# Optimization experiments

Measured on AMD Instinct MI355X. Metric: run time of the kernel, lower is better.

## Reference

```python
import jax, jax.numpy as jnp
import numpy as np

MASK_VALUE = 1.0e6   # mask_value default in get_interpolation
N_NH = 3             # nh_inter: number of nearest neighbors kept by topk
POWER = 2            # inverse-distance weighting power
CUTOFF_DIST = 0.01   # cutoff_dist: distances clamped below this value


def setup_inputs() -> dict:
    key = jax.random.key(0)
    k1, k2, k3 = jax.random.split(key, 3)
    b, n_l, l, nh, nv, f = 1, 4096, 16, 1, 4, 1
    nh_sz, nt = 9, 16            # neighbor cells per cell; target points per cell
    n = n_l * l                  # 65536 fine-grid points
    K = nh_sz * l * nh           # 144 candidate source points per cell
    x = jax.random.normal(k1, (b, n, nh, nv, f), dtype=jnp.float32)
    mask = jnp.zeros((b, n, nh, nv), dtype=jnp.float32)  # 0 = valid point
    dist = jax.random.uniform(k2, (b, n_l, nt, K), dtype=jnp.float32)
    nh_idx = jax.random.randint(k3, (n_l, nh_sz), 0, n_l)  # neighbor-cell table
    return {"x": x, "mask": mask, "dist": dist, "nh_idx": nh_idx}


def reference(x, mask, dist, nh_idx):
    b, n, nh, nv, f = x.shape            # f == 1 (required by original gather layout)
    _, n_l, nt, K = dist.shape
    l = n // n_l
    # --- get_nh: group fine points into coarse cells, gather neighbor cells ---
    x_c = x.reshape(b, n_l, l * nh * nv * f)
    m_c = mask.reshape(b, n_l, l * nh * nv)
    x_nh = x_c[:, nh_idx].reshape(b, n_l, K, nv, f)      # (b,n_l,K,nv,f)
    mask_nh = m_c[:, nh_idx].reshape(b, n_l, K, nv)      # (b,n_l,K,nv)
    # --- masked distances broadcast over target points and variables ---
    dist_m = dist[:, :, :, :, None] + mask_nh[:, :, None, :, :] * MASK_VALUE  # (b,n_l,nt,K,nv)
    dist_m = jnp.moveaxis(dist_m, 3, -1)                 # (b,n_l,nt,nv,K)
    # --- top-k smallest distances (irregular topk) ---
    neg_vals, idx = jax.lax.top_k(-dist_m, N_NH)
    dist_vals = -neg_vals                                # (b,n_l,nt,nv,N_NH)
    # --- gather selected neighbor features ---
    xh = jnp.moveaxis(x_nh[..., 0], 2, -1)               # (b,n_l,nv,K)
    xh = jnp.broadcast_to(xh[:, :, None], (b, n_l, nt, nv, K))
    x_g = jnp.take_along_axis(xh, idx, axis=-1)          # (b,n_l,nt,nv,N_NH)
    # --- inverse-distance weights ---
    dv = jnp.maximum(dist_vals, CUTOFF_DIST)
    w = 1.0 / dv ** POWER
    w = w / w.sum(axis=-1, keepdims=True)
    x_inter = (x_g * w).sum(axis=-1)                     # (b,n_l,nt,nv)
    return x_inter.reshape(b, n_l * nt, nv, f)
```

## Files before the change

### kernel.cpp

```cpp
#include <hip/hip_runtime.h>

#define N_L   4096
#define NT    16
#define NV    4
#define NHSZ  9
#define KCAND 144
#define MASKV 1.0e6f
#define CUT   0.01f
#define BIG   3.0e38f

__global__ __launch_bounds__(256) void flag_kernel(const float* __restrict__ mask,
                                                   int* __restrict__ flags) {
    int gid  = blockIdx.x * 256 + threadIdx.x;
    int cell = gid >> 6;
    int lane = gid & 63;
    if (cell < N_L) {
        float m = mask[cell * 64 + lane];
        unsigned long long b = __ballot(m != 0.0f);
        if (lane == 0) flags[cell] = (b != 0ULL) ? 1 : 0;
    }
}

__global__ __launch_bounds__(256) void interp_kernel(
    const float* __restrict__ x,
    const float* __restrict__ mask,
    const float* __restrict__ dist,
    const int*   __restrict__ nh_idx,
    const int*   __restrict__ flags,
    float*       __restrict__ out)
{
    const int tid = blockIdx.x * 256 + threadIdx.x;
    const int c   = tid >> 4;

    int  cells[NHSZ];
    bool clean = true;
#pragma unroll
    for (int j = 0; j < NHSZ; ++j) {
        cells[j] = nh_idx[c * NHSZ + j];
        clean &= (flags[cells[j]] == 0);
    }

    const float4* dp = (const float4*)(dist + (size_t)tid * KCAND);
    const float4* xc = (const float4*)x;
    const float4* mc = (const float4*)mask;

    float4 result;

    if (clean) {
        float d0 = BIG, d1 = BIG, d2 = BIG;
        int   i0 = 0,   i1 = 0,   i2 = 0;

#pragma unroll 6
        for (int q = 0; q < KCAND / 4; ++q) {
            float4 dd = dp[q];
            const float de[4] = {dd.x, dd.y, dd.z, dd.w};
            const int kb = q * 4;
#pragma unroll
            for (int e = 0; e < 4; ++e) {
                float d = de[e];
                int   k = kb + e;
                bool c0 = d < d0, c1 = d < d1, c2 = d < d2;
                d2 = c1 ? d1 : (c2 ? d : d2);
                i2 = c1 ? i1 : (c2 ? k : i2);
                d1 = c0 ? d0 : (c1 ? d : d1);
                i1 = c0 ? i0 : (c1 ? k : i1);
                d0 = c0 ? d  : d0;
                i0 = c0 ? k  : i0;
            }
        }

        int j0 = i0 >> 4, p0 = i0 & 15;
        int j1 = i1 >> 4, p1 = i1 & 15;
        int j2 = i2 >> 4, p2 = i2 & 15;
        float4 xa = xc[cells[j0] * 16 + p0];
        float4 xb = xc[cells[j1] * 16 + p1];
        float4 xd = xc[cells[j2] * 16 + p2];

        float v0 = fmaxf(d0, CUT), v1 = fmaxf(d1, CUT), v2 = fmaxf(d2, CUT);
        float w0 = 1.0f / (v0 * v0);
        float w1 = 1.0f / (v1 * v1);
        float w2 = 1.0f / (v2 * v2);
        float inv = 1.0f / (w0 + w1 + w2);

        result.x = (xa.x * w0 + xb.x * w1 + xd.x * w2) * inv;
        result.y = (xa.y * w0 + xb.y * w1 + xd.y * w2) * inv;
        result.z = (xa.z * w0 + xb.z * w1 + xd.z * w2) * inv;
        result.w = (xa.w * w0 + xb.w * w1 + xd.w * w2) * inv;
    } else {
        float sd[NV][3];
        int   si[NV][3];
#pragma unroll
        for (int v = 0; v < NV; ++v) {
            sd[v][0] = sd[v][1] = sd[v][2] = BIG;
            si[v][0] = si[v][1] = si[v][2] = 0;
        }
        for (int q = 0; q < KCAND / 4; ++q) {
            float4 dd = dp[q];
            const float de[4] = {dd.x, dd.y, dd.z, dd.w};
#pragma unroll
            for (int e = 0; e < 4; ++e) {
                int k = q * 4 + e;
                int j = k >> 4, p = k & 15;
                float4 m4 = mc[cells[j] * 16 + p];
                const float me[4] = {m4.x, m4.y, m4.z, m4.w};
#pragma unroll
                for (int v = 0; v < NV; ++v) {
                    float dm = fmaf(me[v], MASKV, de[e]);
                    bool c0 = dm < sd[v][0], c1 = dm < sd[v][1], c2 = dm < sd[v][2];
                    sd[v][2] = c1 ? sd[v][1] : (c2 ? dm : sd[v][2]);
                    si[v][2] = c1 ? si[v][1] : (c2 ? k  : si[v][2]);
                    sd[v][1] = c0 ? sd[v][0] : (c1 ? dm : sd[v][1]);
                    si[v][1] = c0 ? si[v][0] : (c1 ? k  : si[v][1]);
                    sd[v][0] = c0 ? dm : sd[v][0];
                    si[v][0] = c0 ? k  : si[v][0];
                }
            }
        }
        float res[NV];
#pragma unroll
        for (int v = 0; v < NV; ++v) {
            float acc = 0.0f, wsum = 0.0f;
#pragma unroll
            for (int s = 0; s < 3; ++s) {
                int k = si[v][s];
                int j = k >> 4, p = k & 15;
                float xv = x[cells[j] * 64 + p * 4 + v];
                float dv = fmaxf(sd[v][s], CUT);
                float w  = 1.0f / (dv * dv);
                acc  += xv * w;
                wsum += w;
            }
            res[v] = acc / wsum;
        }
        result = make_float4(res[0], res[1], res[2], res[3]);
    }

    ((float4*)out)[tid] = result;
}

extern "C" void kernel_launch(void* const* d_in, const int* in_sizes, int n_in,
                              void* d_out, int out_size, void* d_ws, size_t ws_size,
                              hipStream_t stream) {
    const float* x      = (const float*)d_in[0];
    const float* mask   = (const float*)d_in[1];
    const float* dist   = (const float*)d_in[2];
    const int*   nh_idx = (const int*)d_in[3];
    float*       out    = (float*)d_out;
    int*         flags  = (int*)d_ws;

    flag_kernel<<<(N_L * 64) / 256, 256, 0, stream>>>(mask, flags);

    interp_kernel<<<(N_L * NT) / 256, 256, 0, stream>>>(x, mask, dist, nh_idx,
                                                        flags, out);
}
```

Baseline: 88.40 us.

## Split each row across four lanes with shuffle top-3 merge and inline mask check

Each target row is now handled by four threads instead of one. Each thread scans an interleaved quarter of the 144 candidate distances, and the partial top-3 lists are merged with two xor-shuffle rounds using index tie-breaking. The separate flag kernel is removed: each block loads its four cells' neighbor tables into shared memory and sets a per-cell dirty flag from the mask with shared atomics. The aim is better-coalesced dist loads, more threads in flight and one fewer launch. In exchange, each block re-reads neighbor mask data that overlaps between blocks, and the masked path now walks candidates one scalar at a time per variable.

```diff
diff --git a/kernel.cpp b/kernel.cpp
--- a/kernel.cpp
+++ b/kernel.cpp
@@ -9,16 +9,8 @@
 #define CUT   0.01f
 #define BIG   3.0e38f
 
-__global__ __launch_bounds__(256) void flag_kernel(const float* __restrict__ mask,
-                                                   int* __restrict__ flags) {
-    int gid  = blockIdx.x * 256 + threadIdx.x;
-    int cell = gid >> 6;
-    int lane = gid & 63;
-    if (cell < N_L) {
-        float m = mask[cell * 64 + lane];
-        unsigned long long b = __ballot(m != 0.0f);
-        if (lane == 0) flags[cell] = (b != 0ULL) ? 1 : 0;
-    }
+__device__ __forceinline__ bool lex_lt(float da, int ia, float db, int ib) {
+    return (da < db) || ((da == db) && (ia < ib));
 }
 
 __global__ __launch_bounds__(256) void interp_kernel(
@@ -26,116 +18,121 @@
     const float* __restrict__ mask,
     const float* __restrict__ dist,
     const int*   __restrict__ nh_idx,
-    const int*   __restrict__ flags,
     float*       __restrict__ out)
 {
-    const int tid = blockIdx.x * 256 + threadIdx.x;
-    const int c   = tid >> 4;
+    __shared__ int s_cells[4 * NHSZ];
+    __shared__ int s_dirty[4];
 
-    int  cells[NHSZ];
-    bool clean = true;
+    const int t    = threadIdx.x;
+    const int row0 = blockIdx.x * 64;
+    const int c0   = row0 >> 4;
+
+    if (t < 4) s_dirty[t] = 0;
+    if (t < 4 * NHSZ) s_cells[t] = nh_idx[c0 * NHSZ + t];
+    __syncthreads();
+
 #pragma unroll
-    for (int j = 0; j < NHSZ; ++j) {
-        cells[j] = nh_idx[c * NHSZ + j];
-        clean &= (flags[cells[j]] == 0);
+    for (int i = 0; i < 9; ++i) {
+        int f = t + 256 * i;
+        int e = f >> 6;
+        int w = f & 63;
+        float m = mask[s_cells[e] * 64 + w];
+        if (m != 0.0f) atomicOr(&s_dirty[e / 9], 1);
     }
+    __syncthreads();
 
-    const float4* dp = (const float4*)(dist + (size_t)tid * KCAND);
-    const float4* xc = (const float4*)x;
-    const float4* mc = (const float4*)mask;
+    const int row = row0 + (t >> 2);
+    const int sub = t & 3;
+    const int lc  = (t >> 2) >> 4;
+    const int* cells = &s_cells[lc * NHSZ];
 
-    float4 result;
-
-    if (clean) {
+    if (s_dirty[lc] == 0) {
+        const float4* dp = (const float4*)(dist + (size_t)row * KCAND);
         float d0 = BIG, d1 = BIG, d2 = BIG;
         int   i0 = 0,   i1 = 0,   i2 = 0;
-
-#pragma unroll 6
-        for (int q = 0; q < KCAND / 4; ++q) {
-            float4 dd = dp[q];
+#pragma unroll
+        for (int m = 0; m < 9; ++m) {
+            float4 dd = dp[sub + 4 * m];
             const float de[4] = {dd.x, dd.y, dd.z, dd.w};
-            const int kb = q * 4;
+            const int kb = 4 * sub + 16 * m;
 #pragma unroll
             for (int e = 0; e < 4; ++e) {
                 float d = de[e];
                 int   k = kb + e;
-                bool c0 = d < d0, c1 = d < d1, c2 = d < d2;
-                d2 = c1 ? d1 : (c2 ? d : d2);
-                i2 = c1 ? i1 : (c2 ? k : i2);
-                d1 = c0 ? d0 : (c1 ? d : d1);
-                i1 = c0 ? i0 : (c1 ? k : i1);
-                d0 = c0 ? d  : d0;
-                i0 = c0 ? k  : i0;
+                bool c0_ = d < d0, c1_ = d < d1, c2_ = d < d2;
+                d2 = c1_ ? d1 : (c2_ ? d : d2);
+                i2 = c1_ ? i1 : (c2_ ? k : i2);
+                d1 = c0_ ? d0 : (c1_ ? d : d1);
+                i1 = c0_ ? i0 : (c1_ ? k : i1);
+                d0 = c0_ ? d  : d0;
+                i0 = c0_ ? k  : i0;
             }
         }
 
-        int j0 = i0 >> 4, p0 = i0 & 15;
-        int j1 = i1 >> 4, p1 = i1 & 15;
-        int j2 = i2 >> 4, p2 = i2 & 15;
-        float4 xa = xc[cells[j0] * 16 + p0];
-        float4 xb = xc[cells[j1] * 16 + p1];
-        float4 xd = xc[cells[j2] * 16 + p2];
+#pragma unroll
+        for (int mm = 0; mm < 2; ++mm) {
+            const int msk = 1 << mm;
+            float ed0 = __shfl_xor(d0, msk);
+            float ed1 = __shfl_xor(d1, msk);
+            float ed2 = __shfl_xor(d2, msk);
+            int   ei0 = __shfl_xor(i0, msk);
+            int   ei1 = __shfl_xor(i1, msk);
+            int   ei2 = __shfl_xor(i2, msk);
+            bool cA = lex_lt(d0, i0, ed0, ei0);
+            float lo0d = cA ? d0 : ed0;  int lo0i = cA ? i0 : ei0;
+            float hi0d = cA ? ed0 : d0;  int hi0i = cA ? ei0 : i0;
+            bool cB = lex_lt(d1, i1, ed1, ei1);
+            float lo1d = cB ? d1 : ed1;  int lo1i = cB ? i1 : ei1;
+            float hi1d = cB ? ed1 : d1;  int hi1i = cB ? ei1 : i1;
+            bool cC = lex_lt(d2, i2, ed2, ei2);
+            float lo2d = cC ? d2 : ed2;  int lo2i = cC ? i2 : ei2;
+            bool cD = lex_lt(hi0d, hi0i, lo1d, lo1i);
+            float r1d = cD ? hi0d : lo1d; int r1i = cD ? hi0i : lo1i;
+            float t2d = cD ? lo1d : hi0d; int t2i = cD ? lo1i : hi0i;
+            bool cE = lex_lt(t2d, t2i, lo2d, lo2i);
+            float r2d = cE ? t2d : lo2d;  int r2i = cE ? t2i : lo2i;
+            d0 = lo0d; i0 = lo0i;
+            d1 = r1d;  i1 = r1i;
+            d2 = r2d;  i2 = r2i;
+        }
 
         float v0 = fmaxf(d0, CUT), v1 = fmaxf(d1, CUT), v2 = fmaxf(d2, CUT);
         float w0 = 1.0f / (v0 * v0);
         float w1 = 1.0f / (v1 * v1);
         float w2 = 1.0f / (v2 * v2);
         float inv = 1.0f / (w0 + w1 + w2);
-
-        result.x = (xa.x * w0 + xb.x * w1 + xd.x * w2) * inv;
-        result.y = (xa.y * w0 + xb.y * w1 + xd.y * w2) * inv;
-        result.z = (xa.z * w0 + xb.z * w1 + xd.z * w2) * inv;
-        result.w = (xa.w * w0 + xb.w * w1 + xd.w * w2) * inv;
+        int j0 = i0 >> 4, p0 = i0 & 15;
+        int j1 = i1 >> 4, p1 = i1 & 15;
+        int j2 = i2 >> 4, p2 = i2 & 15;
+        float xa = x[cells[j0] * 64 + p0 * 4 + sub];
+        float xb = x[cells[j1] * 64 + p1 * 4 + sub];
+        float xd = x[cells[j2] * 64 + p2 * 4 + sub];
+        out[row * 4 + sub] = (xa * w0 + xb * w1 + xd * w2) * inv;
     } else {
-        float sd[NV][3];
-        int   si[NV][3];
-#pragma unroll
-        for (int v = 0; v < NV; ++v) {
-            sd[v][0] = sd[v][1] = sd[v][2] = BIG;
-            si[v][0] = si[v][1] = si[v][2] = 0;
+        const float* dr = dist + (size_t)row * KCAND;
+        float d0 = BIG, d1 = BIG, d2 = BIG;
+        int   i0 = 0,   i1 = 0,   i2 = 0;
+        for (int k = 0; k < KCAND; ++k) {
+            int j = k >> 4, p = k & 15;
+            float dm = fmaf(mask[cells[j] * 64 + p * 4 + sub], MASKV, dr[k]);
+            bool c0_ = dm < d0, c1_ = dm < d1, c2_ = dm < d2;
+            d2 = c1_ ? d1 : (c2_ ? dm : d2);
+            i2 = c1_ ? i1 : (c2_ ? k  : i2);
+            d1 = c0_ ? d0 : (c1_ ? dm : d1);
+            i1 = c0_ ? i0 : (c1_ ? k  : i1);
+            d0 = c0_ ? dm : d0;
+            i0 = c0_ ? k  : i0;
         }
-        for (int q = 0; q < KCAND / 4; ++q) {
-            float4 dd = dp[q];
-            const float de[4] = {dd.x, dd.y, dd.z, dd.w};
-#pragma unroll
-            for (int e = 0; e < 4; ++e) {
-                int k = q * 4 + e;
-                int j = k >> 4, p = k & 15;
-                float4 m4 = mc[cells[j] * 16 + p];
-                const float me[4] = {m4.x, m4.y, m4.z, m4.w};
-#pragma unroll
-                for (int v = 0; v < NV; ++v) {
-                    float dm = fmaf(me[v], MASKV, de[e]);
-                    bool c0 = dm < sd[v][0], c1 = dm < sd[v][1], c2 = dm < sd[v][2];
-                    sd[v][2] = c1 ? sd[v][1] : (c2 ? dm : sd[v][2]);
-                    si[v][2] = c1 ? si[v][1] : (c2 ? k  : si[v][2]);
-                    sd[v][1] = c0 ? sd[v][0] : (c1 ? dm : sd[v][1]);
-                    si[v][1] = c0 ? si[v][0] : (c1 ? k  : si[v][1]);
-                    sd[v][0] = c0 ? dm : sd[v][0];
-                    si[v][0] = c0 ? k  : si[v][0];
-                }
-            }
-        }
-        float res[NV];
-#pragma unroll
-        for (int v = 0; v < NV; ++v) {
-            float acc = 0.0f, wsum = 0.0f;
-#pragma unroll
-            for (int s = 0; s < 3; ++s) {
-                int k = si[v][s];
-                int j = k >> 4, p = k & 15;
-                float xv = x[cells[j] * 64 + p * 4 + v];
-                float dv = fmaxf(sd[v][s], CUT);
-                float w  = 1.0f / (dv * dv);
-                acc  += xv * w;
-                wsum += w;
-            }
-            res[v] = acc / wsum;
-        }
-        result = make_float4(res[0], res[1], res[2], res[3]);
+        float v0 = fmaxf(d0, CUT), v1 = fmaxf(d1, CUT), v2 = fmaxf(d2, CUT);
+        float w0 = 1.0f / (v0 * v0);
+        float w1 = 1.0f / (v1 * v1);
+        float w2 = 1.0f / (v2 * v2);
+        float inv = 1.0f / (w0 + w1 + w2);
+        float xa = x[cells[i0 >> 4] * 64 + (i0 & 15) * 4 + sub];
+        float xb = x[cells[i1 >> 4] * 64 + (i1 & 15) * 4 + sub];
+        float xd = x[cells[i2 >> 4] * 64 + (i2 & 15) * 4 + sub];
+        out[row * 4 + sub] = (xa * w0 + xb * w1 + xd * w2) * inv;
     }
-
-    ((float4*)out)[tid] = result;
 }
 
 extern "C" void kernel_launch(void* const* d_in, const int* in_sizes, int n_in,
@@ -146,10 +143,7 @@
     const float* dist   = (const float*)d_in[2];
     const int*   nh_idx = (const int*)d_in[3];
     float*       out    = (float*)d_out;
-    int*         flags  = (int*)d_ws;
 
-    flag_kernel<<<(N_L * 64) / 256, 256, 0, stream>>>(mask, flags);
-
-    interp_kernel<<<(N_L * NT) / 256, 256, 0, stream>>>(x, mask, dist, nh_idx,
-                                                        flags, out);
+    interp_kernel<<<(N_L * NT * 4) / 256, 256, 0, stream>>>(x, mask, dist,
+                                                            nh_idx, out);
 }
```

Measured after the change: 88.29 us. No clear change (-0.1%).
